# Kernel tuning notes

Hardware: AMD Instinct MI355X
Metric: run time of the kernel (lower is better)

The kernel has to match this reference:

```python
import jax, jax.numpy as jnp
import numpy as np

N_TOTAL = 2_000_000   # total particles across all events
N_EVENTS = 20_000     # number of events (segments)
H = 64                # phi/rho hidden width
OUT = 10              # output classes


def _lin(x, W, b):
    # torch nn.Linear: y = x @ W.T + b
    return x @ W.T + b


def setup_inputs() -> dict:
    key = jax.random.key(0)
    ks = jax.random.split(key, 24)
    s = 0.1  # small init scale
    inp = {
        "values": jax.random.normal(ks[0], (N_TOTAL,), dtype=jnp.float32),
        "seg_ids": jnp.sort(jax.random.randint(ks[1], (N_TOTAL,), 0, N_EVENTS)),
        "p1w0": jax.random.normal(ks[2], (H, 1), dtype=jnp.float32) * s,
        "p1b0": jax.random.normal(ks[3], (H,), dtype=jnp.float32) * s,
        "p1w1": jax.random.normal(ks[4], (H, H), dtype=jnp.float32) * s,
        "p1b1": jax.random.normal(ks[5], (H,), dtype=jnp.float32) * s,
        "r1w0": jax.random.normal(ks[6], (H, H), dtype=jnp.float32) * s,
        "r1b0": jax.random.normal(ks[7], (H,), dtype=jnp.float32) * s,
        "r1w1": jax.random.normal(ks[8], (H, H), dtype=jnp.float32) * s,
        "r1b1": jax.random.normal(ks[9], (H,), dtype=jnp.float32) * s,
        "o1w": jax.random.normal(ks[10], (H, H), dtype=jnp.float32) * s,
        "o1b": jax.random.normal(ks[11], (H,), dtype=jnp.float32) * s,
        "p2w0": jax.random.normal(ks[12], (H, H), dtype=jnp.float32) * s,
        "p2b0": jax.random.normal(ks[13], (H,), dtype=jnp.float32) * s,
        "p2w1": jax.random.normal(ks[14], (H, H), dtype=jnp.float32) * s,
        "p2b1": jax.random.normal(ks[15], (H,), dtype=jnp.float32) * s,
        "r2w0": jax.random.normal(ks[16], (H, H), dtype=jnp.float32) * s,
        "r2b0": jax.random.normal(ks[17], (H,), dtype=jnp.float32) * s,
        "r2w1": jax.random.normal(ks[18], (H, H), dtype=jnp.float32) * s,
        "r2b1": jax.random.normal(ks[19], (H,), dtype=jnp.float32) * s,
        "o2w": jax.random.normal(ks[20], (OUT, H), dtype=jnp.float32) * s,
        "o2b": jax.random.normal(ks[21], (OUT,), dtype=jnp.float32) * s,
    }
    return inp


def reference(values, seg_ids, p1w0, p1b0, p1w1, p1b1, r1w0, r1b0, r1w1, r1b1,
              o1w, o1b, p2w0, p2b0, p2w1, p2b1, r2w0, r2b0, r2w1, r2b1, o2w, o2b):
    relu = jax.nn.relu
    # stage 1: phi1 on each scalar particle value -> [N, H]
    h = relu(_lin(values[:, None], p1w0, p1b0))
    h = relu(_lin(h, p1w1, p1b1))
    # jagged sum over particles within each event (the inner deepset sum)
    ev = jax.ops.segment_sum(h, seg_ids, num_segments=N_EVENTS)  # [E, H]
    # rho1 + output linear + activation per event
    ev = relu(_lin(ev, r1w0, r1b0))
    ev = relu(_lin(ev, r1w1, r1b1))
    ev = relu(_lin(ev, o1w, o1b))  # [E, H] (output_size of deepset1 = rho_sizes[-1])
    # stage 2: phi2 per event, sum over all events
    h2 = relu(_lin(ev, p2w0, p2b0))
    h2 = relu(_lin(h2, p2w1, p2b1))
    s2 = jnp.sum(h2, axis=0, keepdims=True)  # [1, H]
    r2 = relu(_lin(s2, r2w0, r2b0))
    r2 = relu(_lin(r2, r2w1, r2b1))
    out = _lin(r2, o2w, o2b)  # [1, OUT]
    return jax.nn.log_softmax(out, axis=1)
```

## Files before the change

kernel.cpp:

```cpp
#include <hip/hip_runtime.h>

#define NT 2000000
#define NE 20000
#define NT4 (NT / 4)
#define K1_BLOCKS 2048
#define K1_WAVES (K1_BLOCKS * 4)

using bf16x8 = __attribute__((ext_vector_type(8))) __bf16;
using half8  = __attribute__((ext_vector_type(8))) _Float16;
using half2v = __attribute__((ext_vector_type(2))) _Float16;
using f32x4  = __attribute__((ext_vector_type(4))) float;
using f32x2  = __attribute__((ext_vector_type(2))) float;
using fvec4  = __attribute__((ext_vector_type(4))) float;

__device__ __forceinline__ void load_bsplit(const float* __restrict__ p,
                                            bf16x8& hi, bf16x8& lo) {
    fvec4 a = *(const fvec4*)p;
    fvec4 b = *(const fvec4*)(p + 4);
#pragma unroll
    for (int e = 0; e < 4; e++) {
        float v  = a[e];
        __bf16 h = (__bf16)v;
        hi[e]    = h;
        lo[e]    = (__bf16)(v - (float)h);
        float v2  = b[e];
        __bf16 h2 = (__bf16)v2;
        hi[e + 4] = h2;
        lo[e + 4] = (__bf16)(v2 - (float)h2);
    }
}

__device__ __forceinline__ half8 load_h8(const float* __restrict__ p) {
    fvec4 a = *(const fvec4*)p;
    fvec4 b = *(const fvec4*)(p + 4);
    half8 r;
#pragma unroll
    for (int e = 0; e < 4; e++) {
        r[e]     = (_Float16)a[e];
        r[e + 4] = (_Float16)b[e];
    }
    return r;
}

__global__ __launch_bounds__(256) void k0_offsets(
    const int* __restrict__ seg, int* __restrict__ off, float* __restrict__ s2) {
    if (blockIdx.x == 0 && threadIdx.x < 64) s2[threadIdx.x] = 0.f;
    const int g = blockIdx.x * 256 + threadIdx.x;
    if (g >= NT4) return;
    const int idx4 = g * 4;
    const int4 s = *(const int4*)(seg + idx4);
    int prev = (g == 0) ? -1 : seg[idx4 - 1];
    int vals[4] = {s.x, s.y, s.z, s.w};
#pragma unroll
    for (int k = 0; k < 4; k++) {
        const int cur = vals[k];
        if (cur != prev) {
            for (int e = prev + 1; e <= cur; ++e) off[e] = idx4 + k;
        }
        prev = cur;
    }
    if (idx4 + 3 == NT - 1) {
        for (int e = prev + 1; e <= NE; ++e) off[e] = NT;
    }
}

__global__ __launch_bounds__(256, 4) void k1_phi1(
    const float* __restrict__ values, const int* __restrict__ off,
    const float* __restrict__ w0, const float* __restrict__ b0,
    const float* __restrict__ w1, const float* __restrict__ b1,
    float* __restrict__ ev) {
    const int tid = threadIdx.x;
    const int w   = tid >> 6;
    const int l   = tid & 63;
    const int l15 = l & 15;
    const int l4  = l >> 4;

    half8 Bh[2][4];
#pragma unroll
    for (int kf = 0; kf < 2; kf++)
#pragma unroll
        for (int jf = 0; jf < 4; jf++)
            Bh[kf][jf] = load_h8(w1 + (jf * 16 + l15) * 64 + kf * 32 + l4 * 8);

    half2v w0h[2][4], b0h[2][4];
#pragma unroll
    for (int kf = 0; kf < 2; kf++) {
        const int kb = kf * 32 + l4 * 8;
#pragma unroll
        for (int e2 = 0; e2 < 4; e2++) {
            f32x2 wp = *(const f32x2*)(w0 + kb + 2 * e2);
            f32x2 bp = *(const f32x2*)(b0 + kb + 2 * e2);
            w0h[kf][e2] = half2v{(_Float16)wp[0], (_Float16)wp[1]};
            b0h[kf][e2] = half2v{(_Float16)bp[0], (_Float16)bp[1]};
        }
    }
    f32x4 biasC[4];
#pragma unroll
    for (int jf = 0; jf < 4; jf++) {
        const float bj = b1[jf * 16 + l15];
#pragma unroll
        for (int r = 0; r < 4; r++) biasC[jf][r] = bj;
    }

    const bool bit0 = (l & 16) != 0;
    const bool bit1 = (l & 32) != 0;
    auto reduce4 = [&](const float sj[4]) -> float {
        float send01 = bit0 ? sj[0] : sj[1];
        float keep01 = bit0 ? sj[1] : sj[0];
        float c01 = keep01 + __shfl_xor(send01, 16);
        float send23 = bit0 ? sj[2] : sj[3];
        float keep23 = bit0 ? sj[3] : sj[2];
        float c23 = keep23 + __shfl_xor(send23, 16);
        float send = bit1 ? c01 : c23;
        float keep = bit1 ? c23 : c01;
        return keep + __shfl_xor(send, 32);
    };

    const int wid = blockIdx.x * 4 + w;

    for (int e = wid; e < NE; e += K1_WAVES) {
        const int s = off[e];
        const int t = off[e + 1];
        const int n = t - s;
        float sj[4] = {0.f, 0.f, 0.f, 0.f};

        if (n > 0) {
            const int nblk = (n + 15) >> 4;
            int idx = s + l15;
            _Float16 vcur = (_Float16)((idx < t) ? values[idx] : 0.f);

            for (int b = 0; b < nblk; ++b) {
                const int idxn = s + (b + 1) * 16 + l15;
                const _Float16 vnxt =
                    (_Float16)((b + 1 < nblk && idxn < t) ? values[idxn] : 0.f);

                const half2v vv = {vcur, vcur};
                half8 A0, A1;
#pragma unroll
                for (int e2 = 0; e2 < 4; e2++) {
                    half2v h0 = vv * w0h[0][e2] + b0h[0][e2];
                    half2v h1 = vv * w0h[1][e2] + b0h[1][e2];
                    const _Float16 z = (_Float16)0.f;
                    A0[2 * e2]     = h0[0] > z ? h0[0] : z;
                    A0[2 * e2 + 1] = h0[1] > z ? h0[1] : z;
                    A1[2 * e2]     = h1[0] > z ? h1[0] : z;
                    A1[2 * e2 + 1] = h1[1] > z ? h1[1] : z;
                }

                f32x4 frag[4];
#pragma unroll
                for (int jf = 0; jf < 4; jf++) {
                    f32x4 tt = __builtin_amdgcn_mfma_f32_16x16x32_f16(
                        A0, Bh[0][jf], biasC[jf], 0, 0, 0);
                    tt = __builtin_amdgcn_mfma_f32_16x16x32_f16(
                        A1, Bh[1][jf], tt, 0, 0, 0);
#pragma unroll
                    for (int r = 0; r < 4; r++) frag[jf][r] = fmaxf(tt[r], 0.f);
                }

                const int rem = n - b * 16;
                if (rem >= 16) {
#pragma unroll
                    for (int jf = 0; jf < 4; jf++)
                        sj[jf] += (frag[jf][0] + frag[jf][1]) +
                                  (frag[jf][2] + frag[jf][3]);
                } else {
#pragma unroll
                    for (int r = 0; r < 4; r++) {
                        const bool ok = (l4 * 4 + r) < rem;
#pragma unroll
                        for (int jf = 0; jf < 4; jf++)
                            sj[jf] += ok ? frag[jf][r] : 0.f;
                    }
                }
                vcur = vnxt;
            }
        }
        ev[(size_t)e * 64 + l] = reduce4(sj);
    }
}

__global__ __launch_bounds__(64) void k2_events(
    const float* __restrict__ ev,
    const float* __restrict__ W0, const float* __restrict__ B0,
    const float* __restrict__ W1, const float* __restrict__ B1,
    const float* __restrict__ W2, const float* __restrict__ B2,
    const float* __restrict__ W3, const float* __restrict__ B3,
    const float* __restrict__ W4, const float* __restrict__ B4,
    float* __restrict__ s2) {
    __shared__ __align__(16) __bf16 xt[64 * 72];
    const int l   = threadIdx.x;
    const int l15 = l & 15;
    const int l4  = l >> 4;
    const int ebase = blockIdx.x * 64;

    const float* Ws[5] = {W0, W1, W2, W3, W4};
    const float* Bs[5] = {B0, B1, B2, B3, B4};

    bf16x8 A[4][2];
#pragma unroll
    for (int pf = 0; pf < 4; pf++) {
        const int e = ebase + pf * 16 + l15;
#pragma unroll
        for (int kf = 0; kf < 2; kf++) {
            bf16x8 a;
            if (e < NE) {
                const float* p = ev + (size_t)e * 64 + kf * 32 + l4 * 8;
                fvec4 x = *(const fvec4*)p;
                fvec4 y = *(const fvec4*)(p + 4);
#pragma unroll
                for (int e2 = 0; e2 < 4; e2++) {
                    a[e2]     = (__bf16)x[e2];
                    a[e2 + 4] = (__bf16)y[e2];
                }
            } else {
#pragma unroll
                for (int e2 = 0; e2 < 8; e2++) a[e2] = (__bf16)0.f;
            }
            A[pf][kf] = a;
        }
    }

#pragma unroll
    for (int L = 0; L < 5; L++) {
        bf16x8 Bh[2][4], Bl[2][4];
#pragma unroll
        for (int kf = 0; kf < 2; kf++)
#pragma unroll
            for (int jf = 0; jf < 4; jf++)
                load_bsplit(Ws[L] + (jf * 16 + l15) * 64 + kf * 32 + l4 * 8,
                            Bh[kf][jf], Bl[kf][jf]);

        f32x4 acc[4][4];
#pragma unroll
        for (int jf = 0; jf < 4; jf++) {
            const float bj = Bs[L][jf * 16 + l15];
#pragma unroll
            for (int pf = 0; pf < 4; pf++)
#pragma unroll
                for (int r = 0; r < 4; r++) acc[pf][jf][r] = bj;
        }
#pragma unroll
        for (int kf = 0; kf < 2; kf++)
#pragma unroll
            for (int pf = 0; pf < 4; pf++)
#pragma unroll
                for (int jf = 0; jf < 4; jf++)
                    acc[pf][jf] = __builtin_amdgcn_mfma_f32_16x16x32_bf16(
                        A[pf][kf], Bh[kf][jf], acc[pf][jf], 0, 0, 0);
#pragma unroll
        for (int kf = 0; kf < 2; kf++)
#pragma unroll
            for (int pf = 0; pf < 4; pf++)
#pragma unroll
                for (int jf = 0; jf < 4; jf++)
                    acc[pf][jf] = __builtin_amdgcn_mfma_f32_16x16x32_bf16(
                        A[pf][kf], Bl[kf][jf], acc[pf][jf], 0, 0, 0);

        if (L < 4) {
#pragma unroll
            for (int pf = 0; pf < 4; pf++)
#pragma unroll
                for (int jf = 0; jf < 4; jf++) {
                    const int j = jf * 16 + l15;
#pragma unroll
                    for (int r = 0; r < 4; r++)
                        xt[(pf * 16 + l4 * 4 + r) * 72 + j] =
                            (__bf16)fmaxf(acc[pf][jf][r], 0.f);
                }
#pragma unroll
            for (int pf = 0; pf < 4; pf++)
#pragma unroll
                for (int kf = 0; kf < 2; kf++)
                    A[pf][kf] = *(const bf16x8*)(xt + (pf * 16 + l15) * 72 +
                                                 kf * 32 + l4 * 8);
        } else {
            float sj[4];
#pragma unroll
            for (int jf = 0; jf < 4; jf++) {
                float s = 0.f;
#pragma unroll
                for (int pf = 0; pf < 4; pf++)
#pragma unroll
                    for (int r = 0; r < 4; r++) {
                        const int e = ebase + pf * 16 + l4 * 4 + r;
                        float v = fmaxf(acc[pf][jf][r], 0.f);
                        s += (e < NE) ? v : 0.f;
                    }
                s += __shfl_xor(s, 16);
                s += __shfl_xor(s, 32);
                sj[jf] = s;
            }
            float v = (l4 == 0) ? sj[0] : (l4 == 1) ? sj[1]
                    : (l4 == 2) ? sj[2] : sj[3];
            atomicAdd(s2 + l, v);
        }
    }
}

__global__ __launch_bounds__(64) void k3_final(
    const float* __restrict__ s2,
    const float* __restrict__ W0, const float* __restrict__ B0,
    const float* __restrict__ W1, const float* __restrict__ B1,
    const float* __restrict__ W2, const float* __restrict__ B2,
    float* __restrict__ out) {
    __shared__ __align__(16) float xb[64];
    __shared__ __align__(16) float yb[64];
    __shared__ float ob[10];
    const int l = threadIdx.x;

    xb[l] = s2[l];
    __syncthreads();

    float a = B0[l];
#pragma unroll
    for (int k = 0; k < 16; k++) {
        fvec4 wv = *(const fvec4*)(W0 + l * 64 + k * 4);
        fvec4 xv = *(const fvec4*)(xb + k * 4);
        a += wv[0] * xv[0] + wv[1] * xv[1] + wv[2] * xv[2] + wv[3] * xv[3];
    }
    yb[l] = fmaxf(a, 0.f);
    __syncthreads();

    float b_ = B1[l];
#pragma unroll
    for (int k = 0; k < 16; k++) {
        fvec4 wv = *(const fvec4*)(W1 + l * 64 + k * 4);
        fvec4 xv = *(const fvec4*)(yb + k * 4);
        b_ += wv[0] * xv[0] + wv[1] * xv[1] + wv[2] * xv[2] + wv[3] * xv[3];
    }
    __syncthreads();
    xb[l] = fmaxf(b_, 0.f);
    __syncthreads();

    if (l < 10) {
        float o = B2[l];
#pragma unroll
        for (int k = 0; k < 16; k++) {
            fvec4 wv = *(const fvec4*)(W2 + l * 64 + k * 4);
            fvec4 xv = *(const fvec4*)(xb + k * 4);
            o += wv[0] * xv[0] + wv[1] * xv[1] + wv[2] * xv[2] + wv[3] * xv[3];
        }
        ob[l] = o;
    }
    __syncthreads();
    if (l == 0) {
        float m = ob[0];
#pragma unroll
        for (int i = 1; i < 10; i++) m = fmaxf(m, ob[i]);
        float sum = 0.f;
#pragma unroll
        for (int i = 0; i < 10; i++) sum = sum + expf(ob[i] - m);
        float ls = logf(sum);
#pragma unroll
        for (int i = 0; i < 10; i++) out[i] = ob[i] - m - ls;
    }
}

extern "C" void kernel_launch(void* const* d_in, const int* in_sizes, int n_in,
                              void* d_out, int out_size, void* d_ws, size_t ws_size,
                              hipStream_t stream) {
    const float* values = (const float*)d_in[0];
    const int*   seg    = (const int*)d_in[1];
    const float* p1w0 = (const float*)d_in[2],  *p1b0 = (const float*)d_in[3];
    const float* p1w1 = (const float*)d_in[4],  *p1b1 = (const float*)d_in[5];
    const float* r1w0 = (const float*)d_in[6],  *r1b0 = (const float*)d_in[7];
    const float* r1w1 = (const float*)d_in[8],  *r1b1 = (const float*)d_in[9];
    const float* o1w  = (const float*)d_in[10], *o1b  = (const float*)d_in[11];
    const float* p2w0 = (const float*)d_in[12], *p2b0 = (const float*)d_in[13];
    const float* p2w1 = (const float*)d_in[14], *p2b1 = (const float*)d_in[15];
    const float* r2w0 = (const float*)d_in[16], *r2b0 = (const float*)d_in[17];
    const float* r2w1 = (const float*)d_in[18], *r2b1 = (const float*)d_in[19];
    const float* o2w  = (const float*)d_in[20], *o2b  = (const float*)d_in[21];

    float* ev  = (float*)d_ws;
    float* s2  = ev + (size_t)NE * 64;
    int*   off = (int*)(s2 + 64);

    hipLaunchKernelGGL(k0_offsets, dim3((NT4 + 255) / 256), dim3(256), 0, stream,
                       seg, off, s2);
    hipLaunchKernelGGL(k1_phi1, dim3(K1_BLOCKS), dim3(256), 0, stream,
                       values, off, p1w0, p1b0, p1w1, p1b1, ev);
    hipLaunchKernelGGL(k2_events, dim3((NE + 63) / 64), dim3(64), 0, stream,
                       ev, r1w0, r1b0, r1w1, r1b1, o1w, o1b,
                       p2w0, p2b0, p2w1, p2b1, s2);
    hipLaunchKernelGGL(k3_final, dim3(1), dim3(64), 0, stream,
                       s2, r2w0, r2b0, r2w1, r2b1, o2w, o2b, (float*)d_out);
}
```

Baseline: 76.07 us.

## Interleave two MFMA chains in phi1 and shrink k2 tiles to 16 events

The k1 event loop now processes two 16-particle blocks per iteration with independent accumulators, so two MFMA chains can overlap. It also drops the software-prefetch of the next value and splits the partial tail block into its own masked path. k1 block count is halved, and k2 now handles 16 events per block instead of 64, launching 1250 blocks for more parallelism at the cost of reloading the weights more often. The NE bounds checks in k2 are removed, which relies on NE being divisible by 16.

```diff
diff --git a/kernel.cpp b/kernel.cpp
--- a/kernel.cpp
+++ b/kernel.cpp
@@ -3,8 +3,9 @@
 #define NT 2000000
 #define NE 20000
 #define NT4 (NT / 4)
-#define K1_BLOCKS 2048
+#define K1_BLOCKS 1024
 #define K1_WAVES (K1_BLOCKS * 4)
+#define K2_BLOCKS (NE / 16)
 
 using bf16x8 = __attribute__((ext_vector_type(8))) __bf16;
 using half8  = __attribute__((ext_vector_type(8))) _Float16;
@@ -101,6 +102,47 @@
 #pragma unroll
         for (int r = 0; r < 4; r++) biasC[jf][r] = bj;
     }
+
+    auto buildA = [&](_Float16 v, half8& A0, half8& A1) {
+        const half2v vv = {v, v};
+#pragma unroll
+        for (int e2 = 0; e2 < 4; e2++) {
+            half2v h0 = vv * w0h[0][e2] + b0h[0][e2];
+            half2v h1 = vv * w0h[1][e2] + b0h[1][e2];
+            const _Float16 z = (_Float16)0.f;
+            A0[2 * e2]     = h0[0] > z ? h0[0] : z;
+            A0[2 * e2 + 1] = h0[1] > z ? h0[1] : z;
+            A1[2 * e2]     = h1[0] > z ? h1[0] : z;
+            A1[2 * e2 + 1] = h1[1] > z ? h1[1] : z;
+        }
+    };
+    auto chain = [&](const half8& A0, const half8& A1, float* sj) {
+#pragma unroll
+        for (int jf = 0; jf < 4; jf++) {
+            f32x4 tt = __builtin_amdgcn_mfma_f32_16x16x32_f16(
+                A0, Bh[0][jf], biasC[jf], 0, 0, 0);
+            tt = __builtin_amdgcn_mfma_f32_16x16x32_f16(
+                A1, Bh[1][jf], tt, 0, 0, 0);
+            sj[jf] += (fmaxf(tt[0], 0.f) + fmaxf(tt[1], 0.f)) +
+                      (fmaxf(tt[2], 0.f) + fmaxf(tt[3], 0.f));
+        }
+    };
+    auto chainTail = [&](const half8& A0, const half8& A1, float* sj, int rem) {
+#pragma unroll
+        for (int jf = 0; jf < 4; jf++) {
+            f32x4 tt = __builtin_amdgcn_mfma_f32_16x16x32_f16(
+                A0, Bh[0][jf], biasC[jf], 0, 0, 0);
+            tt = __builtin_amdgcn_mfma_f32_16x16x32_f16(
+                A1, Bh[1][jf], tt, 0, 0, 0);
+            float s = 0.f;
+#pragma unroll
+            for (int r = 0; r < 4; r++) {
+                const bool ok = (l4 * 4 + r) < rem;
+                s += ok ? fmaxf(tt[r], 0.f) : 0.f;
+            }
+            sj[jf] += s;
+        }
+    };
 
     const bool bit0 = (l & 16) != 0;
     const bool bit1 = (l & 32) != 0;
@@ -122,60 +164,40 @@
         const int s = off[e];
         const int t = off[e + 1];
         const int n = t - s;
-        float sj[4] = {0.f, 0.f, 0.f, 0.f};
-
-        if (n > 0) {
-            const int nblk = (n + 15) >> 4;
-            int idx = s + l15;
-            _Float16 vcur = (_Float16)((idx < t) ? values[idx] : 0.f);
-
-            for (int b = 0; b < nblk; ++b) {
-                const int idxn = s + (b + 1) * 16 + l15;
-                const _Float16 vnxt =
-                    (_Float16)((b + 1 < nblk && idxn < t) ? values[idxn] : 0.f);
-
-                const half2v vv = {vcur, vcur};
-                half8 A0, A1;
-#pragma unroll
-                for (int e2 = 0; e2 < 4; e2++) {
-                    half2v h0 = vv * w0h[0][e2] + b0h[0][e2];
-                    half2v h1 = vv * w0h[1][e2] + b0h[1][e2];
-                    const _Float16 z = (_Float16)0.f;
-                    A0[2 * e2]     = h0[0] > z ? h0[0] : z;
-                    A0[2 * e2 + 1] = h0[1] > z ? h0[1] : z;
-                    A1[2 * e2]     = h1[0] > z ? h1[0] : z;
-                    A1[2 * e2 + 1] = h1[1] > z ? h1[1] : z;
-                }
-
-                f32x4 frag[4];
-#pragma unroll
-                for (int jf = 0; jf < 4; jf++) {
-                    f32x4 tt = __builtin_amdgcn_mfma_f32_16x16x32_f16(
-                        A0, Bh[0][jf], biasC[jf], 0, 0, 0);
-                    tt = __builtin_amdgcn_mfma_f32_16x16x32_f16(
-                        A1, Bh[1][jf], tt, 0, 0, 0);
-#pragma unroll
-                    for (int r = 0; r < 4; r++) frag[jf][r] = fmaxf(tt[r], 0.f);
-                }
-
-                const int rem = n - b * 16;
-                if (rem >= 16) {
-#pragma unroll
-                    for (int jf = 0; jf < 4; jf++)
-                        sj[jf] += (frag[jf][0] + frag[jf][1]) +
-                                  (frag[jf][2] + frag[jf][3]);
-                } else {
-#pragma unroll
-                    for (int r = 0; r < 4; r++) {
-                        const bool ok = (l4 * 4 + r) < rem;
-#pragma unroll
-                        for (int jf = 0; jf < 4; jf++)
-                            sj[jf] += ok ? frag[jf][r] : 0.f;
-                    }
-                }
-                vcur = vnxt;
-            }
-        }
+        const int nfull = n >> 4;
+        const float* vp = values + s + l15;
+
+        float sjA[4] = {0.f, 0.f, 0.f, 0.f};
+        float sjB[4] = {0.f, 0.f, 0.f, 0.f};
+
+        int b = 0;
+        for (; b + 2 <= nfull; b += 2) {
+            const _Float16 vA = (_Float16)vp[b * 16];
+            const _Float16 vB = (_Float16)vp[b * 16 + 16];
+            half8 A0A, A1A, A0B, A1B;
+            buildA(vA, A0A, A1A);
+            buildA(vB, A0B, A1B);
+            chain(A0A, A1A, sjA);
+            chain(A0B, A1B, sjB);
+        }
+        if (b < nfull) {
+            const _Float16 vA = (_Float16)vp[b * 16];
+            half8 A0A, A1A;
+            buildA(vA, A0A, A1A);
+            chain(A0A, A1A, sjA);
+        }
+        const int rem = n & 15;
+        if (rem) {
+            const _Float16 vA =
+                (_Float16)((l15 < rem) ? vp[nfull * 16] : 0.f);
+            half8 A0A, A1A;
+            buildA(vA, A0A, A1A);
+            chainTail(A0A, A1A, sjA, rem);
+        }
+
+        float sj[4];
+#pragma unroll
+        for (int jf = 0; jf < 4; jf++) sj[jf] = sjA[jf] + sjB[jf];
         ev[(size_t)e * 64 + l] = reduce4(sj);
     }
 }
@@ -188,37 +210,28 @@
     const float* __restrict__ W3, const float* __restrict__ B3,
     const float* __restrict__ W4, const float* __restrict__ B4,
     float* __restrict__ s2) {
-    __shared__ __align__(16) __bf16 xt[64 * 72];
+    __shared__ __align__(16) __bf16 xt[16 * 72];
     const int l   = threadIdx.x;
     const int l15 = l & 15;
     const int l4  = l >> 4;
-    const int ebase = blockIdx.x * 64;
+    const int ebase = blockIdx.x * 16;
 
     const float* Ws[5] = {W0, W1, W2, W3, W4};
     const float* Bs[5] = {B0, B1, B2, B3, B4};
 
-    bf16x8 A[4][2];
-#pragma unroll
-    for (int pf = 0; pf < 4; pf++) {
-        const int e = ebase + pf * 16 + l15;
-#pragma unroll
-        for (int kf = 0; kf < 2; kf++) {
-            bf16x8 a;
-            if (e < NE) {
-                const float* p = ev + (size_t)e * 64 + kf * 32 + l4 * 8;
-                fvec4 x = *(const fvec4*)p;
-                fvec4 y = *(const fvec4*)(p + 4);
-#pragma unroll
-                for (int e2 = 0; e2 < 4; e2++) {
-                    a[e2]     = (__bf16)x[e2];
-                    a[e2 + 4] = (__bf16)y[e2];
-                }
-            } else {
-#pragma unroll
-                for (int e2 = 0; e2 < 8; e2++) a[e2] = (__bf16)0.f;
-            }
-            A[pf][kf] = a;
-        }
+    bf16x8 A[2];
+#pragma unroll
+    for (int kf = 0; kf < 2; kf++) {
+        const float* p = ev + (size_t)(ebase + l15) * 64 + kf * 32 + l4 * 8;
+        fvec4 x = *(const fvec4*)p;
+        fvec4 y = *(const fvec4*)(p + 4);
+        bf16x8 a;
+#pragma unroll
+        for (int e2 = 0; e2 < 4; e2++) {
+            a[e2]     = (__bf16)x[e2];
+            a[e2 + 4] = (__bf16)y[e2];
+        }
+        A[kf] = a;
     }
 
 #pragma unroll
@@ -231,62 +244,44 @@
                 load_bsplit(Ws[L] + (jf * 16 + l15) * 64 + kf * 32 + l4 * 8,
                             Bh[kf][jf], Bl[kf][jf]);
 
-        f32x4 acc[4][4];
+        f32x4 acc[4];
 #pragma unroll
         for (int jf = 0; jf < 4; jf++) {
             const float bj = Bs[L][jf * 16 + l15];
 #pragma unroll
-            for (int pf = 0; pf < 4; pf++)
-#pragma unroll
-                for (int r = 0; r < 4; r++) acc[pf][jf][r] = bj;
+            for (int r = 0; r < 4; r++) acc[jf][r] = bj;
         }
 #pragma unroll
         for (int kf = 0; kf < 2; kf++)
 #pragma unroll
-            for (int pf = 0; pf < 4; pf++)
-#pragma unroll
-                for (int jf = 0; jf < 4; jf++)
-                    acc[pf][jf] = __builtin_amdgcn_mfma_f32_16x16x32_bf16(
-                        A[pf][kf], Bh[kf][jf], acc[pf][jf], 0, 0, 0);
+            for (int jf = 0; jf < 4; jf++)
+                acc[jf] = __builtin_amdgcn_mfma_f32_16x16x32_bf16(
+                    A[kf], Bh[kf][jf], acc[jf], 0, 0, 0);
 #pragma unroll
         for (int kf = 0; kf < 2; kf++)
 #pragma unroll
-            for (int pf = 0; pf < 4; pf++)
-#pragma unroll
-                for (int jf = 0; jf < 4; jf++)
-                    acc[pf][jf] = __builtin_amdgcn_mfma_f32_16x16x32_bf16(
-                        A[pf][kf], Bl[kf][jf], acc[pf][jf], 0, 0, 0);
+            for (int jf = 0; jf < 4; jf++)
+                acc[jf] = __builtin_amdgcn_mfma_f32_16x16x32_bf16(
+                    A[kf], Bl[kf][jf], acc[jf], 0, 0, 0);
 
         if (L < 4) {
 #pragma unroll
-            for (int pf = 0; pf < 4; pf++)
-#pragma unroll
-                for (int jf = 0; jf < 4; jf++) {
-                    const int j = jf * 16 + l15;
-#pragma unroll
-                    for (int r = 0; r < 4; r++)
-                        xt[(pf * 16 + l4 * 4 + r) * 72 + j] =
-                            (__bf16)fmaxf(acc[pf][jf][r], 0.f);
-                }
-#pragma unroll
-            for (int pf = 0; pf < 4; pf++)
-#pragma unroll
-                for (int kf = 0; kf < 2; kf++)
-                    A[pf][kf] = *(const bf16x8*)(xt + (pf * 16 + l15) * 72 +
-                                                 kf * 32 + l4 * 8);
+            for (int jf = 0; jf < 4; jf++) {
+                const int j = jf * 16 + l15;
+#pragma unroll
+                for (int r = 0; r < 4; r++)
+                    xt[(l4 * 4 + r) * 72 + j] =
+                        (__bf16)fmaxf(acc[jf][r], 0.f);
+            }
+#pragma unroll
+            for (int kf = 0; kf < 2; kf++)
+                A[kf] = *(const bf16x8*)(xt + l15 * 72 + kf * 32 + l4 * 8);
         } else {
             float sj[4];
 #pragma unroll
             for (int jf = 0; jf < 4; jf++) {
-                float s = 0.f;
-#pragma unroll
-                for (int pf = 0; pf < 4; pf++)
-#pragma unroll
-                    for (int r = 0; r < 4; r++) {
-                        const int e = ebase + pf * 16 + l4 * 4 + r;
-                        float v = fmaxf(acc[pf][jf][r], 0.f);
-                        s += (e < NE) ? v : 0.f;
-                    }
+                float s = (fmaxf(acc[jf][0], 0.f) + fmaxf(acc[jf][1], 0.f)) +
+                          (fmaxf(acc[jf][2], 0.f) + fmaxf(acc[jf][3], 0.f));
                 s += __shfl_xor(s, 16);
                 s += __shfl_xor(s, 32);
                 sj[jf] = s;
@@ -381,7 +376,7 @@
                        seg, off, s2);
     hipLaunchKernelGGL(k1_phi1, dim3(K1_BLOCKS), dim3(256), 0, stream,
                        values, off, p1w0, p1b0, p1w1, p1b1, ev);
-    hipLaunchKernelGGL(k2_events, dim3((NE + 63) / 64), dim3(64), 0, stream,
+    hipLaunchKernelGGL(k2_events, dim3(K2_BLOCKS), dim3(64), 0, stream,
                        ev, r1w0, r1b0, r1w1, r1b1, o1w, o1b,
                        p2w0, p2b0, p2w1, p2b1, s2);
     hipLaunchKernelGGL(k3_final, dim3(1), dim3(64), 0, stream,
```

After: 89.93 us. 18.2% more time.
